# Optimization experiments

Measured on AMD Instinct MI355X. Metric: run time of the kernel, lower is better.

Reference implementation:

```python
import jax, jax.numpy as jnp
import numpy as np

B, S, D, E, K = 4, 2048, 1024, 8, 2
DF = 4 * D


def setup_inputs() -> dict:
    key = jax.random.key(0)
    ks = jax.random.split(key, 7)
    x = jax.random.normal(ks[0], (B, S, D), dtype=jnp.float32)
    Wr = jax.random.normal(ks[1], (D, E), dtype=jnp.float32) * 0.02
    br = jnp.zeros((E,), dtype=jnp.float32)
    W1 = jax.random.normal(ks[2], (E, D, DF), dtype=jnp.float32) * 0.02
    b1 = jnp.zeros((E, DF), dtype=jnp.float32)
    W2 = jax.random.normal(ks[3], (E, DF, D), dtype=jnp.float32) * 0.02
    b2 = jnp.zeros((E, D), dtype=jnp.float32)
    return {"x": x, "Wr": Wr, "br": br, "W1": W1, "b1": b1, "W2": W2, "b2": b2}


def reference(x, Wr, br, W1, b1, W2, b2):
    # Router: softmax gates then top-k
    gates = jax.nn.softmax(x @ Wr + br, axis=-1)               # [B,S,E]
    topk_vals, topk_idx = jax.lax.top_k(gates, K)              # [B,S,K]

    # Per-(token, expert) combine weight: gate value if expert selected else 0
    onehot = jax.nn.one_hot(topk_idx, E, dtype=gates.dtype)    # [B,S,K,E]
    combine = jnp.sum(onehot * topk_vals[..., None], axis=2)   # [B,S,E]

    # Expert MLPs (loop over fixed small expert count, fully vectorized per expert)
    output = jnp.zeros_like(x)
    for e in range(E):
        h = jax.nn.gelu(x @ W1[e] + b1[e], approximate=False)  # [B,S,4D]
        y = h @ W2[e] + b2[e]                                  # [B,S,D]
        output = output + combine[..., e:e + 1] * y

    # Load-balancing aux loss (dispatch mask: 1.0 where expert selected)
    dispatch = jnp.max(onehot, axis=2)                         # [B,S,E]
    mean_gates = gates.mean(axis=(0, 1))
    mean_dispatch = dispatch.mean(axis=(0, 1))
    aux_loss = jnp.sum(mean_gates * mean_dispatch) * E / (B * S)
    return output, aux_loss
```

## Files before the change

### kernel.cpp

```cpp
#include <hip/hip_runtime.h>
#include <hip/hip_bf16.h>
#include <hip/hip_fp16.h>

typedef _Float16 f16;
typedef _Float16 half8 __attribute__((ext_vector_type(8)));
typedef _Float16 half4 __attribute__((ext_vector_type(4)));
typedef float   floatx4 __attribute__((ext_vector_type(4)));

#define N_TOK   8192
#define D_DIM   1024
#define E_NUM   8
#define DF_DIM  4096
#define MAX_SLOTS 18432
#define MAX_RT    72

#define MI_COUNT  0
#define MI_CURSOR 8
#define MI_OFF    16
#define MI_TOTAL  25
#define MI_RTE    26
#define MI_SUMG   168

__device__ __forceinline__ void gld_lds16(const void* g, void* l) {
    __builtin_amdgcn_global_load_lds(
        (__attribute__((address_space(1))) const void*)g,
        (__attribute__((address_space(3))) void*)l, 16, 0, 0);
}

__device__ __forceinline__ float gelu_f(float v) {
    float u = 0.7978845608028654f * v * (1.0f + 0.044715f * v * v);
    float t = __expf(-2.0f * fabsf(u));
    float th = (1.0f - t) / (1.0f + t);
    th = (u >= 0.f) ? th : -th;
    return 0.5f * v * (1.0f + th);
}

__global__ __launch_bounds__(256) void convert_x_kernel(
    const float* __restrict__ x, f16* __restrict__ xh)
{
    int idx = blockIdx.x * 256 + threadIdx.x;
    const int stride = gridDim.x * 256;
    const int n4 = (N_TOK * D_DIM) / 4;
    for (int i = idx; i < n4; i += stride) {
        float4 v = ((const float4*)x)[i];
        half4 o = { (f16)v.x, (f16)v.y, (f16)v.z, (f16)v.w };
        ((half4*)xh)[i] = o;
    }
}

__global__ __launch_bounds__(256) void transpose_conv_kernel(
    const float* __restrict__ src, f16* __restrict__ dst, int R, int C)
{
    const float* s = src + (size_t)blockIdx.z * R * C;
    f16* d = dst + (size_t)blockIdx.z * R * C;
    __shared__ float tile[64 * 65];
    const int rb = blockIdx.y * 64, cb = blockIdx.x * 64;
    const int tid = threadIdx.x;
#pragma unroll
    for (int j = 0; j < 4; ++j) {
        int lin = j * 1024 + tid * 4;
        int r = lin >> 6, c = lin & 63;
        float4 v = *(const float4*)(s + (size_t)(rb + r) * C + (cb + c));
        tile[r * 65 + c + 0] = v.x; tile[r * 65 + c + 1] = v.y;
        tile[r * 65 + c + 2] = v.z; tile[r * 65 + c + 3] = v.w;
    }
    __syncthreads();
#pragma unroll
    for (int j = 0; j < 4; ++j) {
        int lin = j * 1024 + tid * 4;
        int c = lin >> 6, r = lin & 63;
        half4 o = { (f16)tile[(r + 0) * 65 + c], (f16)tile[(r + 1) * 65 + c],
                    (f16)tile[(r + 2) * 65 + c], (f16)tile[(r + 3) * 65 + c] };
        *(half4*)(d + (size_t)(cb + c) * R + (rb + r)) = o;
    }
}

__global__ __launch_bounds__(256) void router_kernel(
    const float* __restrict__ x, const float* __restrict__ Wr,
    const float* __restrict__ br,
    int* __restrict__ topk_idx, float* __restrict__ topk_w,
    int* __restrict__ meta)
{
    const int w = threadIdx.x >> 6, l = threadIdx.x & 63;
    __shared__ float blk_sg[E_NUM];
    __shared__ int   blk_cnt[E_NUM];
    if (threadIdx.x < E_NUM) { blk_sg[threadIdx.x] = 0.f; blk_cnt[threadIdx.x] = 0; }
    __syncthreads();

    for (int it = 0; it < 4; ++it) {
        const int t = blockIdx.x * 16 + w * 4 + it;
        const float* xr = x + (size_t)t * D_DIM + l * 16;
        float acc[E_NUM] = {0.f,0.f,0.f,0.f,0.f,0.f,0.f,0.f};
#pragma unroll
        for (int i = 0; i < 16; i += 4) {
            float4 xv = *(const float4*)(xr + i);
            const float xs[4] = {xv.x, xv.y, xv.z, xv.w};
#pragma unroll
            for (int jj = 0; jj < 4; ++jj) {
                int d = l * 16 + i + jj;
                float4 w0 = *(const float4*)(Wr + (size_t)d * 8);
                float4 w1 = *(const float4*)(Wr + (size_t)d * 8 + 4);
                acc[0] += xs[jj] * w0.x; acc[1] += xs[jj] * w0.y;
                acc[2] += xs[jj] * w0.z; acc[3] += xs[jj] * w0.w;
                acc[4] += xs[jj] * w1.x; acc[5] += xs[jj] * w1.y;
                acc[6] += xs[jj] * w1.z; acc[7] += xs[jj] * w1.w;
            }
        }
#pragma unroll
        for (int e = 0; e < E_NUM; ++e) {
#pragma unroll
            for (int off = 32; off > 0; off >>= 1)
                acc[e] += __shfl_down(acc[e], off);
        }
        if (l == 0) {
            float lg[E_NUM], g[E_NUM];
            float mx = -1e30f;
#pragma unroll
            for (int e = 0; e < E_NUM; ++e) { lg[e] = acc[e] + br[e]; mx = fmaxf(mx, lg[e]); }
            float sum = 0.f;
#pragma unroll
            for (int e = 0; e < E_NUM; ++e) { g[e] = __expf(lg[e] - mx); sum += g[e]; }
            float inv = 1.f / sum;
#pragma unroll
            for (int e = 0; e < E_NUM; ++e) g[e] *= inv;
            int e1 = 0; float v1 = g[0];
#pragma unroll
            for (int e = 1; e < E_NUM; ++e) if (g[e] > v1) { v1 = g[e]; e1 = e; }
            int e2 = -1; float v2 = -1.f;
#pragma unroll
            for (int e = 0; e < E_NUM; ++e) if (e != e1 && g[e] > v2) { v2 = g[e]; e2 = e; }
            topk_idx[t * 2 + 0] = e1; topk_idx[t * 2 + 1] = e2;
            topk_w[t * 2 + 0] = v1;   topk_w[t * 2 + 1] = v2;
#pragma unroll
            for (int e = 0; e < E_NUM; ++e) atomicAdd(&blk_sg[e], g[e]);
            atomicAdd(&blk_cnt[e1], 1); atomicAdd(&blk_cnt[e2], 1);
        }
    }
    __syncthreads();
    if (threadIdx.x < E_NUM) {
        atomicAdd((float*)(meta + MI_SUMG) + threadIdx.x, blk_sg[threadIdx.x]);
        atomicAdd(meta + MI_COUNT + threadIdx.x, blk_cnt[threadIdx.x]);
    }
}

__global__ void scan_kernel(int* __restrict__ meta, float* __restrict__ out_aux)
{
    if (threadIdx.x != 0 || blockIdx.x != 0) return;
    int off = 0;
    for (int e = 0; e < E_NUM; ++e) {
        meta[MI_OFF + e] = off;
        int cnt = meta[MI_COUNT + e];
        int padded = ((cnt + 255) >> 8) << 8;
        for (int rt = off >> 8; rt < (off + padded) >> 8; ++rt)
            meta[MI_RTE + rt] = e;
        off += padded;
    }
    meta[MI_OFF + E_NUM] = off;
    meta[MI_TOTAL] = off >> 8;
    const float* sg = (const float*)(meta + MI_SUMG);
    float aux = 0.f;
    for (int e = 0; e < E_NUM; ++e)
        aux += (sg[e] / (float)N_TOK) * ((float)meta[MI_COUNT + e] / (float)N_TOK);
    out_aux[0] = aux * (float)E_NUM / (float)N_TOK;
}

__global__ __launch_bounds__(256) void fill_kernel(
    const int* __restrict__ topk_idx, const float* __restrict__ topk_w,
    int* __restrict__ meta, int* __restrict__ slot_token, float* __restrict__ slot_weight,
    int* __restrict__ slot_of)
{
    int t = blockIdx.x * 256 + threadIdx.x;
#pragma unroll
    for (int k = 0; k < 2; ++k) {
        int e = topk_idx[t * 2 + k];
        int p = atomicAdd(meta + MI_CURSOR + e, 1);
        int slot = meta[MI_OFF + e] + p;
        slot_token[slot] = t;
        slot_weight[slot] = topk_w[t * 2 + k];
        slot_of[t * 2 + k] = slot;
    }
}


#define STAGE_HALF(T, H) do {                                                  \
    f16* ld_ = smem + ((T)&1)*32768 + ((H)&1)*16384 + ((H)>>1)*8192;           \
    const f16* s0_ = ((H)&1) ? bsrc[((H)>>1)*2]     : asrc[((H)>>1)*2];        \
    const f16* s1_ = ((H)&1) ? bsrc[((H)>>1)*2 + 1] : asrc[((H)>>1)*2 + 1];    \
    gld_lds16(s0_ + (size_t)(T)*64, ld_ + tid*8);                              \
    gld_lds16(s1_ + (size_t)(T)*64, ld_ + 4096 + tid*8);                       \
} while(0)

#define READ_A(MH) do {                                                        \
    _Pragma("unroll")                                                          \
    for (int mj = 0; mj < 4; ++mj) {                                           \
        const f16* pa_ = LA + (size_t)(rA + (MH)*64 + mj*16) * 64;             \
        af[mj][0] = *(const half8*)(pa_ + sw0);                                \
        af[mj][1] = *(const half8*)(pa_ + sw1);                                \
    }                                                                          \
} while(0)

#define READ_B(NH) do {                                                        \
    _Pragma("unroll")                                                          \
    for (int nj = 0; nj < 2; ++nj) {                                           \
        const f16* pb_ = LB + (size_t)(rB + (NH)*32 + nj*16) * 64;             \
        bf[NH][nj][0] = *(const half8*)(pb_ + sw0);                            \
        bf[NH][nj][1] = *(const half8*)(pb_ + sw1);                            \
    }                                                                          \
} while(0)

#define MFMA_Q(MH, NH) do {                                                    \
    __builtin_amdgcn_s_setprio(1);                                             \
    _Pragma("unroll")                                                          \
    for (int mj = 0; mj < 4; ++mj)                                             \
    { _Pragma("unroll")                                                        \
      for (int nj = 0; nj < 2; ++nj) {                                         \
        acc[(MH)*4+mj][(NH)*2+nj] = __builtin_amdgcn_mfma_f32_16x16x32_f16(    \
            af[mj][0], bf[NH][nj][0], acc[(MH)*4+mj][(NH)*2+nj], 0, 0, 0);     \
        acc[(MH)*4+mj][(NH)*2+nj] = __builtin_amdgcn_mfma_f32_16x16x32_f16(    \
            af[mj][1], bf[NH][nj][1], acc[(MH)*4+mj][(NH)*2+nj], 0, 0, 0);     \
      } }                                                                      \
    __builtin_amdgcn_s_setprio(0);                                             \
} while(0)

template<int KD, int NCOLS, int KSPLIT, bool GATHER, bool GELU, bool BIAS>
__global__ __launch_bounds__(512, 2) void gemm256_kernel(
    const f16* __restrict__ A, const f16* __restrict__ Bw,
    const float* __restrict__ bias, const int* __restrict__ slot_token,
    const int* __restrict__ meta, f16* __restrict__ Out, size_t out_kp_stride)
{
    constexpr int KLOC = KD / KSPLIT;
    constexpr int NT = KLOC / 64;
    __shared__ __align__(16) f16 smem[65536];

    const int rt = blockIdx.y;
    if (rt >= meta[MI_TOTAL]) return;
    const int e  = meta[MI_RTE + rt];
    const int nt = blockIdx.x;
    const int kp = blockIdx.z;
    const int kbase = kp * KLOC;

    const int tid = threadIdx.x;
    const int w = tid >> 6, l = tid & 63;
    const int wr2 = w >> 2, wc2 = w & 3;
    const int fr = l & 15, fq = l >> 4;

    const int srow = tid >> 3;
    const int kcs  = (tid & 7) ^ (srow & 7);

    const f16* asrc[4]; const f16* bsrc[4];
#pragma unroll
    for (int i = 0; i < 4; ++i) {
        int r = ((i >> 1) * 128) + ((i & 1) * 64) + srow;
        int ar;
        if (GATHER) ar = slot_token[rt * 256 + r];
        else        ar = rt * 256 + r;
        asrc[i] = A + (size_t)ar * KD + kbase + kcs * 8;
        bsrc[i] = Bw + ((size_t)e * NCOLS + (size_t)nt * 256 + r) * KD + kbase + kcs * 8;
    }

    const int rA  = wr2 * 128 + fr;
    const int rB  = wc2 * 64 + fr;
    const int sw0 = ( fq      ^ (fr & 7)) * 8;
    const int sw1 = ((4 + fq) ^ (fr & 7)) * 8;

    floatx4 acc[8][4];
#pragma unroll
    for (int m = 0; m < 8; ++m)
#pragma unroll
        for (int n = 0; n < 4; ++n) acc[m][n] = (floatx4){0.f, 0.f, 0.f, 0.f};

    half8 af[4][2];
    half8 bf[2][2][2];

    STAGE_HALF(0, 0); STAGE_HALF(0, 1); STAGE_HALF(0, 2); STAGE_HALF(0, 3);
    if (NT > 1) { STAGE_HALF(1, 0); STAGE_HALF(1, 1); STAGE_HALF(1, 2); }
    asm volatile("s_waitcnt vmcnt(6)" ::: "memory");
    __builtin_amdgcn_s_barrier();

#pragma unroll 2
    for (int t = 0; t < NT; ++t) {
        const f16* LA = smem + (t & 1) * 32768;
        const f16* LB = LA + 16384;
        READ_A(0); READ_B(0);
        if (t > 0 && t + 1 < NT) { STAGE_HALF(t + 1, 1); STAGE_HALF(t + 1, 2); }
        __builtin_amdgcn_s_barrier();
        MFMA_Q(0, 0);
        __builtin_amdgcn_s_barrier();
        READ_B(1);
        if (t + 1 < NT) STAGE_HALF(t + 1, 3);
        __builtin_amdgcn_s_barrier();
        MFMA_Q(0, 1);
        __builtin_amdgcn_s_barrier();
        READ_A(1);
        __builtin_amdgcn_s_barrier();
        MFMA_Q(1, 0);
        __builtin_amdgcn_s_barrier();
        if (t + 2 < NT) STAGE_HALF(t + 2, 0);
        __builtin_amdgcn_s_barrier();
        MFMA_Q(1, 1);
        if (t + 1 < NT) {
            if (t + 1 < NT - 1) asm volatile("s_waitcnt vmcnt(2)" ::: "memory");
            else                asm volatile("s_waitcnt vmcnt(0)" ::: "memory");
            __builtin_amdgcn_s_barrier();
        }
    }

    f16* Op = Out + (size_t)kp * out_kp_stride;
    const int orow0 = rt * 256 + wr2 * 128;
    const int ocol0 = nt * 256 + wc2 * 64;
#pragma unroll
    for (int mi = 0; mi < 8; ++mi) {
#pragma unroll
        for (int n = 0; n < 4; ++n) {
            const int col = ocol0 + n * 16 + fr;
            float bs = 0.f;
            if (BIAS) bs = bias[(size_t)e * NCOLS + col];
#pragma unroll
            for (int j = 0; j < 4; ++j) {
                const int row = orow0 + mi * 16 + fq * 4 + j;
                float v = acc[mi][n][j] + bs;
                if (GELU) v = gelu_f(v);
                Op[(size_t)row * NCOLS + col] = (f16)v;
            }
        }
    }
}

__global__ __launch_bounds__(256) void combine_kernel(
    const f16* __restrict__ P, const int* __restrict__ slot_of,
    const int* __restrict__ topk_idx, const float* __restrict__ topk_w,
    const float* __restrict__ b2, float* __restrict__ out)
{
    const int t = blockIdx.x;
    const int c = threadIdx.x;
    const size_t PS = (size_t)MAX_SLOTS * D_DIM;
    const int s0 = slot_of[t * 2], s1 = slot_of[t * 2 + 1];
    const int e0 = topk_idx[t * 2], e1 = topk_idx[t * 2 + 1];
    const float w0 = topk_w[t * 2], w1 = topk_w[t * 2 + 1];
    half4 a0 = *(const half4*)(P + (size_t)s0 * D_DIM + c * 4);
    half4 a1 = *(const half4*)(P + PS + (size_t)s0 * D_DIM + c * 4);
    half4 c0 = *(const half4*)(P + (size_t)s1 * D_DIM + c * 4);
    half4 c1 = *(const half4*)(P + PS + (size_t)s1 * D_DIM + c * 4);
    float4 bb0 = *(const float4*)(b2 + (size_t)e0 * D_DIM + c * 4);
    float4 bb1 = *(const float4*)(b2 + (size_t)e1 * D_DIM + c * 4);
    float4 o;
    o.x = w0 * ((float)a0[0] + (float)a1[0] + bb0.x) + w1 * ((float)c0[0] + (float)c1[0] + bb1.x);
    o.y = w0 * ((float)a0[1] + (float)a1[1] + bb0.y) + w1 * ((float)c0[1] + (float)c1[1] + bb1.y);
    o.z = w0 * ((float)a0[2] + (float)a1[2] + bb0.z) + w1 * ((float)c0[2] + (float)c1[2] + bb1.z);
    o.w = w0 * ((float)a0[3] + (float)a1[3] + bb0.w) + w1 * ((float)c0[3] + (float)c1[3] + bb1.w);
    *(float4*)(out + (size_t)t * D_DIM + c * 4) = o;
}

extern "C" void kernel_launch(void* const* d_in, const int* in_sizes, int n_in,
                              void* d_out, int out_size, void* d_ws, size_t ws_size,
                              hipStream_t stream) {
    const float* x  = (const float*)d_in[0];
    const float* Wr = (const float*)d_in[1];
    const float* br = (const float*)d_in[2];
    const float* W1 = (const float*)d_in[3];
    const float* b1 = (const float*)d_in[4];
    const float* W2 = (const float*)d_in[5];
    const float* b2 = (const float*)d_in[6];
    float* out = (float*)d_out;

    char* ws = (char*)d_ws;
    const size_t SZ_XH  = (size_t)N_TOK * D_DIM * 2;
    const size_t SZ_W1T = (size_t)E_NUM * DF_DIM * D_DIM * 2;
    const size_t SZ_W2T = SZ_W1T;
    const size_t SZ_H   = (size_t)MAX_SLOTS * DF_DIM * 2;

    f16* xh  = (f16*)(ws);
    f16* W1t = (f16*)(ws + SZ_XH);
    f16* W2t = (f16*)(ws + SZ_XH + SZ_W1T);
    f16* H   = (f16*)(ws + SZ_XH + SZ_W1T + SZ_W2T);
    f16* P   = (f16*)ws;
    char* p  = ws + SZ_XH + SZ_W1T + SZ_W2T + SZ_H;
    int*   topk_idx    = (int*)p;    p += (size_t)N_TOK * 2 * 4;
    float* topk_w      = (float*)p;  p += (size_t)N_TOK * 2 * 4;
    int*   slot_token  = (int*)p;    p += (size_t)MAX_SLOTS * 4;
    float* slot_weight = (float*)p;  p += (size_t)MAX_SLOTS * 4;
    int*   slot_of     = (int*)p;    p += (size_t)N_TOK * 2 * 4;
    int*   meta        = (int*)p;

    hipMemsetAsync(slot_token, 0, (size_t)MAX_SLOTS * 8 + (size_t)N_TOK * 2 * 4 + 1024, stream);

    convert_x_kernel<<<2048, 256, 0, stream>>>(x, xh);
    transpose_conv_kernel<<<dim3(DF_DIM / 64, D_DIM / 64, E_NUM), 256, 0, stream>>>(W1, W1t, D_DIM, DF_DIM);
    transpose_conv_kernel<<<dim3(D_DIM / 64, DF_DIM / 64, E_NUM), 256, 0, stream>>>(W2, W2t, DF_DIM, D_DIM);
    router_kernel<<<N_TOK / 16, 256, 0, stream>>>(x, Wr, br, topk_idx, topk_w, meta);
    scan_kernel<<<1, 64, 0, stream>>>(meta, out + (size_t)N_TOK * D_DIM);
    fill_kernel<<<N_TOK / 256, 256, 0, stream>>>(topk_idx, topk_w, meta, slot_token, slot_weight, slot_of);

    gemm256_kernel<D_DIM, DF_DIM, 1, true, true, true>
        <<<dim3(DF_DIM / 256, MAX_RT, 1), 512, 0, stream>>>(
        xh, W1t, b1, slot_token, meta, H, 0);

    gemm256_kernel<DF_DIM, D_DIM, 2, false, false, false>
        <<<dim3(D_DIM / 256, MAX_RT, 2), 512, 0, stream>>>(
        H, W2t, nullptr, slot_token, meta, P, (size_t)MAX_SLOTS * D_DIM);

    combine_kernel<<<N_TOK, 256, 0, stream>>>(P, slot_of, topk_idx, topk_w, b2, out);

    (void)in_sizes; (void)n_in; (void)ws_size;
}
```

Before: 619.3 us.

## Load all LDS fragments upfront and drop most intra-iteration barriers in GEMM loop

The main GEMM loop now reads both A halves and both B halves from LDS at the start of each k-tile into a doubled A fragment array, then issues all four MFMA quadrants back to back. The many s_barrier calls between quadrants are removed, leaving one barrier after an lgkmcnt wait before restaging the buffer for tile t+2. The prologue stages less ahead, and stages 1 to 3 of the next tile are issued at the top of the iteration. This aims to cut synchronisation overhead and let MFMAs run uninterrupted, at the cost of more VGPRs for fragments and different load/compute interleaving that may pressure occupancy under launch_bounds(512,2).

```diff
diff --git a/kernel.cpp b/kernel.cpp
--- a/kernel.cpp
+++ b/kernel.cpp
@@ -194,8 +194,8 @@
     _Pragma("unroll")                                                          \
     for (int mj = 0; mj < 4; ++mj) {                                           \
         const f16* pa_ = LA + (size_t)(rA + (MH)*64 + mj*16) * 64;             \
-        af[mj][0] = *(const half8*)(pa_ + sw0);                                \
-        af[mj][1] = *(const half8*)(pa_ + sw1);                                \
+        af[MH][mj][0] = *(const half8*)(pa_ + sw0);                            \
+        af[MH][mj][1] = *(const half8*)(pa_ + sw1);                            \
     }                                                                          \
 } while(0)
 
@@ -215,9 +215,9 @@
     { _Pragma("unroll")                                                        \
       for (int nj = 0; nj < 2; ++nj) {                                         \
         acc[(MH)*4+mj][(NH)*2+nj] = __builtin_amdgcn_mfma_f32_16x16x32_f16(    \
-            af[mj][0], bf[NH][nj][0], acc[(MH)*4+mj][(NH)*2+nj], 0, 0, 0);     \
+            af[MH][mj][0], bf[NH][nj][0], acc[(MH)*4+mj][(NH)*2+nj], 0, 0, 0); \
         acc[(MH)*4+mj][(NH)*2+nj] = __builtin_amdgcn_mfma_f32_16x16x32_f16(    \
-            af[mj][1], bf[NH][nj][1], acc[(MH)*4+mj][(NH)*2+nj], 0, 0, 0);     \
+            af[MH][mj][1], bf[NH][nj][1], acc[(MH)*4+mj][(NH)*2+nj], 0, 0, 0); \
       } }                                                                      \
     __builtin_amdgcn_s_setprio(0);                                             \
 } while(0)
@@ -269,34 +269,28 @@
 #pragma unroll
         for (int n = 0; n < 4; ++n) acc[m][n] = (floatx4){0.f, 0.f, 0.f, 0.f};
 
-    half8 af[4][2];
+    half8 af[2][4][2];
     half8 bf[2][2][2];
 
     STAGE_HALF(0, 0); STAGE_HALF(0, 1); STAGE_HALF(0, 2); STAGE_HALF(0, 3);
-    if (NT > 1) { STAGE_HALF(1, 0); STAGE_HALF(1, 1); STAGE_HALF(1, 2); }
-    asm volatile("s_waitcnt vmcnt(6)" ::: "memory");
+    if (NT > 1) STAGE_HALF(1, 0);
+    asm volatile("s_waitcnt vmcnt(2)" ::: "memory");
     __builtin_amdgcn_s_barrier();
 
 #pragma unroll 2
     for (int t = 0; t < NT; ++t) {
         const f16* LA = smem + (t & 1) * 32768;
         const f16* LB = LA + 16384;
-        READ_A(0); READ_B(0);
-        if (t > 0 && t + 1 < NT) { STAGE_HALF(t + 1, 1); STAGE_HALF(t + 1, 2); }
-        __builtin_amdgcn_s_barrier();
+        if (t + 1 < NT) { STAGE_HALF(t + 1, 1); STAGE_HALF(t + 1, 2); STAGE_HALF(t + 1, 3); }
+        READ_A(0); READ_B(0); READ_B(1); READ_A(1);
         MFMA_Q(0, 0);
-        __builtin_amdgcn_s_barrier();
-        READ_B(1);
-        if (t + 1 < NT) STAGE_HALF(t + 1, 3);
-        __builtin_amdgcn_s_barrier();
         MFMA_Q(0, 1);
-        __builtin_amdgcn_s_barrier();
-        READ_A(1);
-        __builtin_amdgcn_s_barrier();
         MFMA_Q(1, 0);
-        __builtin_amdgcn_s_barrier();
-        if (t + 2 < NT) STAGE_HALF(t + 2, 0);
-        __builtin_amdgcn_s_barrier();
+        if (t + 2 < NT) {
+            asm volatile("s_waitcnt lgkmcnt(0)" ::: "memory");
+            __builtin_amdgcn_s_barrier();
+            STAGE_HALF(t + 2, 0);
+        }
         MFMA_Q(1, 1);
         if (t + 1 < NT) {
             if (t + 1 < NT - 1) asm volatile("s_waitcnt vmcnt(2)" ::: "memory");
```

Result: no change. 617.8 us (-0.2%).
